# Kernel optimization log

Hardware: AMD Instinct MI355X
Metric: run time of the kernel (lower is better)

The kernel has to match this reference:

```python
import jax, jax.numpy as jnp
import numpy as np

WINDOW = 7
HEADS = 16
DIM_HEAD = 32
SCALE = DIM_HEAD ** -0.5


def _rel_pos_indices(window: int) -> np.ndarray:
    # Static relative-position index table, shape [w*w, w*w], values in [0, (2w-1)^2)
    wdiff = 2 * window - 1
    axis = np.arange(window)
    grid = np.stack(np.meshgrid(axis, axis, indexing='ij'), -1).reshape(-1, 2)  # [w*w, 2]
    pos = grid[:, None, :] - grid[None, :, :]
    pos -= pos.min()
    return pos @ np.array([wdiff, 1])


_IDX = jnp.asarray(_rel_pos_indices(WINDOW))  # [49, 49]


def setup_inputs() -> dict:
    key = jax.random.key(0)
    k1, k2, k3, k4 = jax.random.split(key, 4)
    dim = 512
    x = jax.random.normal(k1, (16, 196, 49, dim), dtype=jnp.float32)
    w_qkv = jax.random.normal(k2, (dim, 3 * dim), dtype=jnp.float32) * 0.02
    bias_table = jax.random.normal(k3, ((2 * WINDOW - 1) ** 2, HEADS), dtype=jnp.float32) * 0.02
    w_out = jax.random.normal(k4, (dim, dim), dtype=jnp.float32) * 0.02
    return {"x": x, "w_qkv": w_qkv, "bias_table": bias_table, "w_out": w_out}


def reference(x, w_qkv, bias_table, w_out):
    b, w, i, dim = x.shape  # [B, nWindows, 49, dim]
    # QKV projection: '... i (s h d) -> s ... h i d'
    qkv = (x @ w_qkv).reshape(b, w, i, 3, HEADS, DIM_HEAD)
    qkv = jnp.transpose(qkv, (3, 0, 1, 4, 2, 5))  # [3, B, W, H, i, d]
    q, k, v = qkv[0], qkv[1], qkv[2]
    # Relative position bias: [H, 49, 49]
    bias = jnp.transpose(bias_table[_IDX], (2, 0, 1))
    sim = jnp.einsum('bwhid,bwhjd->bwhij', q, k) * SCALE + bias
    attn = jax.nn.softmax(sim, axis=-1)
    out = jnp.einsum('bwhij,bwhjd->bwhid', attn, v)
    # '... h i d -> ... i (h d)' then output projection (no bias)
    out = jnp.transpose(out, (0, 1, 3, 2, 4)).reshape(b, w, i, dim)
    return out @ w_out
```

## Files before the change

kernel.cpp:

```cpp
#include <hip/hip_runtime.h>
#include <hip/hip_bf16.h>

typedef unsigned short u16;
typedef __attribute__((ext_vector_type(8))) short bf16x8;
typedef __attribute__((ext_vector_type(4))) float f32x4;
typedef __attribute__((ext_vector_type(8))) unsigned short u16x8;

#define MFMA16 __builtin_amdgcn_mfma_f32_16x16x32_bf16

__device__ inline u16 f2bf(float f) {
    union { float f; unsigned u; } v; v.f = f;
    unsigned u = v.u;
    u += 0x7fffu + ((u >> 16) & 1u);
    return (u16)(u >> 16);
}

__device__ __forceinline__ void gl_lds16(const u16* g, u16* l) {
    __builtin_amdgcn_global_load_lds(
        (const __attribute__((address_space(1))) unsigned int*)g,
        (__attribute__((address_space(3))) unsigned int*)l, 16, 0, 0);
}

__global__ __launch_bounds__(256) void cast_kernel(const float* __restrict__ in,
                                                   u16* __restrict__ out, int n8) {
    int i = blockIdx.x * 256 + threadIdx.x;
    if (i >= n8) return;
    const float4* p4 = (const float4*)in;
    float4 a = p4[2 * (size_t)i], b = p4[2 * (size_t)i + 1];
    u16x8 o;
    o[0] = f2bf(a.x); o[1] = f2bf(a.y); o[2] = f2bf(a.z); o[3] = f2bf(a.w);
    o[4] = f2bf(b.x); o[5] = f2bf(b.y); o[6] = f2bf(b.z); o[7] = f2bf(b.w);
    *(u16x8*)(out + 8 * (size_t)i) = o;
}

__global__ __launch_bounds__(256) void castT_kernel(const float* __restrict__ in,
                                                    u16* __restrict__ out, int N, int total) {
    int i = blockIdx.x * 256 + threadIdx.x;
    if (i >= total) return;
    int n = i >> 9, k = i & 511;
    out[i] = f2bf(in[(size_t)k * N + n]);
}

template <int OUT_BF16>
__global__ __launch_bounds__(256) void gemm_bt_kernel(const u16* __restrict__ A,
                                                      const u16* __restrict__ Bt,
                                                      void* __restrict__ Cv,
                                                      int M, int N, int K) {
    __shared__ __align__(16) u16 As[128 * 32];
    __shared__ __align__(16) u16 Bs[128 * 32];

    const int tid  = threadIdx.x;
    const int lane = tid & 63;
    const int wave = tid >> 6;
    const int l16  = lane & 15;
    const int quad = lane >> 4;
    const int wm   = (wave >> 1) * 64;
    const int wn   = (wave & 1) * 64;
    const int n0   = blockIdx.x * 128;
    const int m0   = blockIdx.y * 128;
    const bool full = (m0 + 128 <= M);

    f32x4 acc[4][4];
#pragma unroll
    for (int i = 0; i < 4; i++)
#pragma unroll
        for (int j = 0; j < 4; j++) acc[i][j] = (f32x4){0.f, 0.f, 0.f, 0.f};

    for (int kk = 0; kk < K; kk += 32) {
        if (full) {
#pragma unroll
            for (int p = 0; p < 2; p++) {
                int idx = tid + p * 256;
                int r = idx >> 2, c = (idx & 3) << 3;
                gl_lds16(A + (size_t)(m0 + r) * K + kk + c, As + idx * 8);
                gl_lds16(Bt + (size_t)(n0 + r) * K + kk + c, Bs + idx * 8);
            }
        } else {
#pragma unroll
            for (int p = 0; p < 2; p++) {
                int idx = tid + p * 256;
                int r = idx >> 2, c = (idx & 3) << 3;
                u16x8 v = {0, 0, 0, 0, 0, 0, 0, 0};
                if (m0 + r < M) v = *(const u16x8*)(A + (size_t)(m0 + r) * K + kk + c);
                *(u16x8*)(As + idx * 8) = v;
                gl_lds16(Bt + (size_t)(n0 + r) * K + kk + c, Bs + idx * 8);
            }
        }
        __syncthreads();

        bf16x8 af[4], bfr[4];
#pragma unroll
        for (int mt = 0; mt < 4; mt++)
            af[mt] = *(const bf16x8*)(&As[(wm + mt * 16 + l16) * 32 + quad * 8]);
#pragma unroll
        for (int nt = 0; nt < 4; nt++)
            bfr[nt] = *(const bf16x8*)(&Bs[(wn + nt * 16 + l16) * 32 + quad * 8]);
#pragma unroll
        for (int mt = 0; mt < 4; mt++)
#pragma unroll
            for (int nt = 0; nt < 4; nt++)
                acc[mt][nt] = MFMA16(af[mt], bfr[nt], acc[mt][nt], 0, 0, 0);
        __syncthreads();
    }

#pragma unroll
    for (int mt = 0; mt < 4; mt++) {
#pragma unroll
        for (int nt = 0; nt < 4; nt++) {
#pragma unroll
            for (int r = 0; r < 4; r++) {
                int gm = m0 + wm + mt * 16 + quad * 4 + r;
                int gn = n0 + wn + nt * 16 + l16;
                if (gm < M) {
                    if (OUT_BF16)
                        ((u16*)Cv)[(size_t)gm * N + gn] = f2bf(acc[mt][nt][r]);
                    else
                        ((float*)Cv)[(size_t)gm * N + gn] = acc[mt][nt][r];
                }
            }
        }
    }
}

__global__ __launch_bounds__(64) void attn_kernel(const u16* __restrict__ qkv,
                                                  const float* __restrict__ bias_table,
                                                  u16* __restrict__ aout) {
    __shared__ __align__(16) u16 Pm[64 * 72];
    __shared__ __align__(16) u16 VmT[32 * 72];
    __shared__ float Bi[176];

    const int lane = threadIdx.x;
    const int l16  = lane & 15;
    const int quad = lane >> 4;
    const int h    = blockIdx.x & 15;
    const int bw   = blockIdx.x >> 4;
    const size_t qb = (size_t)bw * 49 * 1536 + h * 32;
    const size_t ob = (size_t)bw * 49 * 512 + h * 32;

    for (int t = lane; t < 169; t += 64) Bi[t] = bias_table[t * 16 + h];
    for (int t = lane; t < 32 * 16; t += 64) {
        int d = t >> 4, tok = 48 + (t & 15);
        VmT[d * 72 + tok] = 0;
    }

    const bf16x8 z8 = {0, 0, 0, 0, 0, 0, 0, 0};
    const f32x4 zf = {0.f, 0.f, 0.f, 0.f};

    bf16x8 qf[4], kf[4];
#pragma unroll
    for (int t = 0; t < 4; t++) {
        int m = t * 16 + l16;
        bool v = m < 49;
        qf[t] = v ? *(const bf16x8*)(qkv + qb + (size_t)m * 1536 + quad * 8) : z8;
        kf[t] = v ? *(const bf16x8*)(qkv + qb + 512 + (size_t)m * 1536 + quad * 8) : z8;
        if (v) {
            u16x8 v8 = *(const u16x8*)(qkv + qb + 1024 + (size_t)m * 1536 + quad * 8);
#pragma unroll
            for (int jj = 0; jj < 8; jj++) VmT[(quad * 8 + jj) * 72 + m] = v8[jj];
        }
    }

    f32x4 s[4][4];
#pragma unroll
    for (int mt = 0; mt < 4; mt++)
#pragma unroll
        for (int nt = 0; nt < 4; nt++) s[mt][nt] = MFMA16(qf[mt], kf[nt], zf, 0, 0, 0);

#pragma unroll
    for (int nt = 0; nt < 4; nt++) {
        int j = nt * 16 + l16;
        int rj = j / 7, cj = j - rj * 7;
#pragma unroll
        for (int mt = 0; mt < 4; mt++) {
#pragma unroll
            for (int r = 0; r < 4; r++) {
                int i = mt * 16 + quad * 4 + r;
                if (j >= 49) {
                    s[mt][nt][r] = -1e30f;
                } else {
                    float val = s[mt][nt][r] * 0.17677669529663687f;
                    if (i < 49) {
                        int ri = i / 7, ci = i - ri * 7;
                        val += Bi[(ri - rj + 6) * 13 + (ci - cj + 6)];
                    }
                    s[mt][nt][r] = val;
                }
            }
        }
    }

    float rsum[4][4];
#pragma unroll
    for (int mt = 0; mt < 4; mt++) {
#pragma unroll
        for (int r = 0; r < 4; r++) {
            float mx = fmaxf(fmaxf(s[mt][0][r], s[mt][1][r]), fmaxf(s[mt][2][r], s[mt][3][r]));
#pragma unroll
            for (int d = 1; d < 16; d <<= 1) mx = fmaxf(mx, __shfl_xor(mx, d, 64));
            float sum = 0.f;
#pragma unroll
            for (int nt = 0; nt < 4; nt++) {
                float e = __expf(s[mt][nt][r] - mx);
                s[mt][nt][r] = e;
                sum += e;
            }
#pragma unroll
            for (int d = 1; d < 16; d <<= 1) sum += __shfl_xor(sum, d, 64);
            rsum[mt][r] = sum;
            int row = mt * 16 + quad * 4 + r;
#pragma unroll
            for (int nt = 0; nt < 4; nt++)
                Pm[row * 72 + nt * 16 + l16] = f2bf(s[mt][nt][r]);
        }
    }
    __syncthreads();

    bf16x8 vf[2][2];
#pragma unroll
    for (int ks = 0; ks < 2; ks++)
#pragma unroll
        for (int nt = 0; nt < 2; nt++)
            vf[ks][nt] = *(const bf16x8*)(&VmT[(nt * 16 + l16) * 72 + ks * 32 + quad * 8]);

    f32x4 o[4][2];
#pragma unroll
    for (int mt = 0; mt < 4; mt++) { o[mt][0] = zf; o[mt][1] = zf; }
#pragma unroll
    for (int mt = 0; mt < 4; mt++) {
#pragma unroll
        for (int ks = 0; ks < 2; ks++) {
            bf16x8 p = *(const bf16x8*)(&Pm[(mt * 16 + l16) * 72 + ks * 32 + quad * 8]);
            o[mt][0] = MFMA16(p, vf[ks][0], o[mt][0], 0, 0, 0);
            o[mt][1] = MFMA16(p, vf[ks][1], o[mt][1], 0, 0, 0);
        }
    }

#pragma unroll
    for (int mt = 0; mt < 4; mt++) {
#pragma unroll
        for (int r = 0; r < 4; r++) {
            int i = mt * 16 + quad * 4 + r;
            if (i < 49) {
                float inv = 1.f / rsum[mt][r];
#pragma unroll
                for (int nt = 0; nt < 2; nt++)
                    aout[ob + (size_t)i * 512 + nt * 16 + l16] = f2bf(o[mt][nt][r] * inv);
            }
        }
    }
}

extern "C" void kernel_launch(void* const* d_in, const int* in_sizes, int n_in,
                              void* d_out, int out_size, void* d_ws, size_t ws_size,
                              hipStream_t stream) {
    const float* x          = (const float*)d_in[0];
    const float* w_qkv      = (const float*)d_in[1];
    const float* bias_table = (const float*)d_in[2];
    const float* w_out      = (const float*)d_in[3];
    float* out = (float*)d_out;

    char* ws = (char*)d_ws;
    u16* xb    = (u16*)ws;
    u16* qkvb  = (u16*)(ws + 157351936LL);
    u16* wqkvT = (u16*)(ws + 157351936LL + 472055808LL);
    u16* woutT = (u16*)(ws + 157351936LL + 472055808LL + 1572864LL);
    u16* aob   = xb;

    cast_kernel<<<38416, 256, 0, stream>>>(x, xb, 9834496);
    castT_kernel<<<3072, 256, 0, stream>>>(w_qkv, wqkvT, 1536, 786432);
    castT_kernel<<<1024, 256, 0, stream>>>(w_out, woutT, 512, 262144);

    gemm_bt_kernel<1><<<dim3(12, 1201), 256, 0, stream>>>(xb, wqkvT, qkvb, 153664, 1536, 512);

    attn_kernel<<<50176, 64, 0, stream>>>(qkvb, bias_table, aob);

    gemm_bt_kernel<0><<<dim3(4, 1201), 256, 0, stream>>>(aob, woutT, out, 153664, 512, 512);
}
```

Before: 1.299 ms.

## Replace GEMM with 256x256 double-buffered swizzled LDS pipeline and XCD remap

Both projection GEMMs move from 128x128 tiles with a K-step of 32 and full-sync single buffering to 256x256 tiles with 8 waves, a K-step of 64, and double-buffered LDS. The next tile's loads are issued in quarters between MFMA phases, and a fixed vmcnt budget, XOR-swizzled LDS addresses, setprio around the MFMA bursts and a block-to-XCD remap are added. The aim is to raise MFMA density, hide global-load latency and cut LDS bank conflicts and redundant global traffic. The cost is much larger LDS use (128KB per block) and higher register pressure. The hand-tuned waitcnt counts also depend on the exact load ordering.

```diff
diff --git a/kernel.cpp b/kernel.cpp
--- a/kernel.cpp
+++ b/kernel.cpp
@@ -7,6 +7,8 @@
 typedef __attribute__((ext_vector_type(8))) unsigned short u16x8;
 
 #define MFMA16 __builtin_amdgcn_mfma_f32_16x16x32_bf16
+#define SB0() __builtin_amdgcn_sched_barrier(0)
+#define BARRIER() do { SB0(); __builtin_amdgcn_s_barrier(); SB0(); } while (0)
 
 __device__ inline u16 f2bf(float f) {
     union { float f; unsigned u; } v; v.f = f;
@@ -41,81 +43,159 @@
     out[i] = f2bf(in[(size_t)k * N + n]);
 }
 
+
+__device__ __forceinline__ bf16x8 lds_frag(const u16* tile, int row, int colbyte) {
+    int off = (row << 7) + colbyte;
+    off ^= ((off >> 9) & 1) << 5;
+    return *(const bf16x8*)((const char*)tile + off);
+}
+
+__device__ __forceinline__ void stage_half(const u16* __restrict__ X, int K,
+                                           int row0, int cap, int k0,
+                                           int lrow, int lcol, u16* half_, int tid) {
+    int r0 = row0 + lrow;      if (r0 > cap) r0 = cap;
+    int r1 = row0 + lrow + 64; if (r1 > cap) r1 = cap;
+    gl_lds16(X + (size_t)r0 * K + k0 + lcol, half_ + tid * 8);
+    gl_lds16(X + (size_t)r1 * K + k0 + lcol, half_ + (tid + 512) * 8);
+}
+
+#define QUAD_MFMA(mhh, nhh)                                                    \
+    _Pragma("unroll") for (int mf2 = 0; mf2 < 4; mf2++)                        \
+    _Pragma("unroll") for (int nf2 = 0; nf2 < 2; nf2++)                        \
+    _Pragma("unroll") for (int ks = 0; ks < 2; ks++)                           \
+        acc[(mhh)*4 + mf2][(nhh)*2 + nf2] =                                    \
+            MFMA16(a[mf2*2 + ks], b[((nhh)*2 + nf2)*2 + ks],                   \
+                   acc[(mhh)*4 + mf2][(nhh)*2 + nf2], 0, 0, 0);
+
+#define LOAD_B_ALL()                                                           \
+    _Pragma("unroll") for (int nf = 0; nf < 4; nf++)                           \
+    _Pragma("unroll") for (int ks = 0; ks < 2; ks++)                           \
+        b[nf*2 + ks] = lds_frag(Btl, wn*64 + nf*16 + l16, ks*64 + quad*16);
+
+#define LOAD_A(mhh)                                                            \
+    _Pragma("unroll") for (int mf2 = 0; mf2 < 4; mf2++)                        \
+    _Pragma("unroll") for (int ks = 0; ks < 2; ks++)                           \
+        a[mf2*2 + ks] = lds_frag(At, wm*128 + (mhh)*64 + mf2*16 + l16,         \
+                                 ks*64 + quad*16);
+
 template <int OUT_BF16>
-__global__ __launch_bounds__(256) void gemm_bt_kernel(const u16* __restrict__ A,
-                                                      const u16* __restrict__ Bt,
-                                                      void* __restrict__ Cv,
-                                                      int M, int N, int K) {
-    __shared__ __align__(16) u16 As[128 * 32];
-    __shared__ __align__(16) u16 Bs[128 * 32];
+__global__ __launch_bounds__(512, 2) void gemm256_kernel(const u16* __restrict__ A,
+                                                         const u16* __restrict__ Bt,
+                                                         void* __restrict__ Cv,
+                                                         int M, int N, int K) {
+    __shared__ __align__(1024) u16 As[2][16384];
+    __shared__ __align__(1024) u16 Bs[2][16384];
 
     const int tid  = threadIdx.x;
     const int lane = tid & 63;
     const int wave = tid >> 6;
     const int l16  = lane & 15;
     const int quad = lane >> 4;
-    const int wm   = (wave >> 1) * 64;
-    const int wn   = (wave & 1) * 64;
-    const int n0   = blockIdx.x * 128;
-    const int m0   = blockIdx.y * 128;
-    const bool full = (m0 + 128 <= M);
-
-    f32x4 acc[4][4];
-#pragma unroll
-    for (int i = 0; i < 4; i++)
+    const int wm   = wave >> 2;
+    const int wn   = wave & 3;
+
+    const int tN = N >> 8;
+    const int nwg = gridDim.x;
+    const int orig = blockIdx.x;
+    const int q = nwg >> 3, r = nwg & 7;
+    const int xcd = orig & 7, lo = orig >> 3;
+    const int wg = (xcd < r ? xcd * (q + 1) : r * (q + 1) + (xcd - r) * q) + lo;
+    const int m0 = (wg / tN) << 8;
+    const int n0 = (wg % tN) << 8;
+
+    const int NT = K >> 6;
+    const int mcap = M - 1;
+    const int ncap = N - 1;
+
+    const int soff  = tid << 4;
+    const int soff2 = soff ^ (((soff >> 9) & 1) << 5);
+    const int lrow  = soff2 >> 7;
+    const int lcol  = (soff2 & 127) >> 1;
+
+    stage_half(Bt, K, n0,       ncap, 0, lrow, lcol, &Bs[0][0],    tid);
+    stage_half(Bt, K, n0 + 128, ncap, 0, lrow, lcol, &Bs[0][8192], tid);
+    stage_half(A,  K, m0,       mcap, 0, lrow, lcol, &As[0][0],    tid);
+    stage_half(A,  K, m0 + 128, mcap, 0, lrow, lcol, &As[0][8192], tid);
+    if (NT > 1) {
+        stage_half(Bt, K, n0,       ncap, 64, lrow, lcol, &Bs[1][0],    tid);
+        stage_half(Bt, K, n0 + 128, ncap, 64, lrow, lcol, &Bs[1][8192], tid);
+        stage_half(A,  K, m0,       mcap, 64, lrow, lcol, &As[1][0],    tid);
+    }
+
+    f32x4 acc[8][4];
+#pragma unroll
+    for (int i = 0; i < 8; i++)
 #pragma unroll
         for (int j = 0; j < 4; j++) acc[i][j] = (f32x4){0.f, 0.f, 0.f, 0.f};
 
-    for (int kk = 0; kk < K; kk += 32) {
-        if (full) {
-#pragma unroll
-            for (int p = 0; p < 2; p++) {
-                int idx = tid + p * 256;
-                int r = idx >> 2, c = (idx & 3) << 3;
-                gl_lds16(A + (size_t)(m0 + r) * K + kk + c, As + idx * 8);
-                gl_lds16(Bt + (size_t)(n0 + r) * K + kk + c, Bs + idx * 8);
-            }
-        } else {
-#pragma unroll
-            for (int p = 0; p < 2; p++) {
-                int idx = tid + p * 256;
-                int r = idx >> 2, c = (idx & 3) << 3;
-                u16x8 v = {0, 0, 0, 0, 0, 0, 0, 0};
-                if (m0 + r < M) v = *(const u16x8*)(A + (size_t)(m0 + r) * K + kk + c);
-                *(u16x8*)(As + idx * 8) = v;
-                gl_lds16(Bt + (size_t)(n0 + r) * K + kk + c, Bs + idx * 8);
-            }
-        }
-        __syncthreads();
-
-        bf16x8 af[4], bfr[4];
-#pragma unroll
-        for (int mt = 0; mt < 4; mt++)
-            af[mt] = *(const bf16x8*)(&As[(wm + mt * 16 + l16) * 32 + quad * 8]);
-#pragma unroll
-        for (int nt = 0; nt < 4; nt++)
-            bfr[nt] = *(const bf16x8*)(&Bs[(wn + nt * 16 + l16) * 32 + quad * 8]);
-#pragma unroll
-        for (int mt = 0; mt < 4; mt++)
-#pragma unroll
-            for (int nt = 0; nt < 4; nt++)
-                acc[mt][nt] = MFMA16(af[mt], bfr[nt], acc[mt][nt], 0, 0, 0);
-        __syncthreads();
-    }
-
-#pragma unroll
-    for (int mt = 0; mt < 4; mt++) {
-#pragma unroll
-        for (int nt = 0; nt < 4; nt++) {
-#pragma unroll
-            for (int r = 0; r < 4; r++) {
-                int gm = m0 + wm + mt * 16 + quad * 4 + r;
-                int gn = n0 + wn + nt * 16 + l16;
-                if (gm < M) {
+    if (NT > 1) asm volatile("s_waitcnt vmcnt(6)");
+    else        asm volatile("s_waitcnt vmcnt(0)");
+    BARRIER();
+
+    for (int t = 0; t < NT; ++t) {
+        const u16* At  = &As[t & 1][0];
+        const u16* Btl = &Bs[t & 1][0];
+        bf16x8 a[8], b[8];
+
+        LOAD_B_ALL();
+        LOAD_A(0);
+        if (t + 1 < NT)
+            stage_half(A, K, m0 + 128, mcap, (t + 1) * 64, lrow, lcol,
+                       &As[(t + 1) & 1][8192], tid);
+        BARRIER();
+        asm volatile("s_waitcnt lgkmcnt(0)");
+        SB0();
+        __builtin_amdgcn_s_setprio(1);
+        QUAD_MFMA(0, 0);
+        __builtin_amdgcn_s_setprio(0);
+        BARRIER();
+
+        if (t + 2 < NT)
+            stage_half(Bt, K, n0, ncap, (t + 2) * 64, lrow, lcol, &Bs[t & 1][0], tid);
+        BARRIER();
+        __builtin_amdgcn_s_setprio(1);
+        QUAD_MFMA(0, 1);
+        __builtin_amdgcn_s_setprio(0);
+        BARRIER();
+
+        LOAD_A(1);
+        if (t + 2 < NT)
+            stage_half(Bt, K, n0 + 128, ncap, (t + 2) * 64, lrow, lcol,
+                       &Bs[t & 1][8192], tid);
+        BARRIER();
+        asm volatile("s_waitcnt lgkmcnt(0)");
+        SB0();
+        __builtin_amdgcn_s_setprio(1);
+        QUAD_MFMA(1, 0);
+        __builtin_amdgcn_s_setprio(0);
+        BARRIER();
+
+        if (t + 2 < NT)
+            stage_half(A, K, m0, mcap, (t + 2) * 64, lrow, lcol, &As[t & 1][0], tid);
+        BARRIER();
+        __builtin_amdgcn_s_setprio(1);
+        QUAD_MFMA(1, 1);
+        __builtin_amdgcn_s_setprio(0);
+        if (t + 1 < NT) {
+            if (t + 2 < NT) asm volatile("s_waitcnt vmcnt(6)");
+            else            asm volatile("s_waitcnt vmcnt(0)");
+        }
+        BARRIER();
+    }
+
+#pragma unroll
+    for (int mf = 0; mf < 8; mf++) {
+#pragma unroll
+        for (int rr = 0; rr < 4; rr++) {
+            int gm = m0 + wm * 128 + mf * 16 + quad * 4 + rr;
+            if (gm < M) {
+#pragma unroll
+                for (int nf = 0; nf < 4; nf++) {
+                    int gn = n0 + wn * 64 + nf * 16 + l16;
                     if (OUT_BF16)
-                        ((u16*)Cv)[(size_t)gm * N + gn] = f2bf(acc[mt][nt][r]);
+                        ((u16*)Cv)[(size_t)gm * N + gn] = f2bf(acc[mf][nf][rr]);
                     else
-                        ((float*)Cv)[(size_t)gm * N + gn] = acc[mt][nt][r];
+                        ((float*)Cv)[(size_t)gm * N + gn] = acc[mf][nf][rr];
                 }
             }
         }
@@ -270,9 +350,9 @@
     castT_kernel<<<3072, 256, 0, stream>>>(w_qkv, wqkvT, 1536, 786432);
     castT_kernel<<<1024, 256, 0, stream>>>(w_out, woutT, 512, 262144);
 
-    gemm_bt_kernel<1><<<dim3(12, 1201), 256, 0, stream>>>(xb, wqkvT, qkvb, 153664, 1536, 512);
+    gemm256_kernel<1><<<dim3(601 * 6), 512, 0, stream>>>(xb, wqkvT, qkvb, 153664, 1536, 512);
 
     attn_kernel<<<50176, 64, 0, stream>>>(qkvb, bias_table, aob);
 
-    gemm_bt_kernel<0><<<dim3(4, 1201), 256, 0, stream>>>(aob, woutT, out, 153664, 512, 512);
-}
+    gemm256_kernel<0><<<dim3(601 * 2), 512, 0, stream>>>(aob, woutT, out, 153664, 512, 512);
+}
```

Result: faster. 1.227 ms (-5.6%).
